# Kernel optimization log

Measured on AMD Instinct MI355X. Metric: run time of the kernel, lower is better.

Reference implementation:

```python
import jax, jax.numpy as jnp
import numpy as np


def _patches3x3(x):
    # x: [B,H,W,C] -> [B,H,W,9,C], SAME zero padding, patch index k = i*3+j
    B, H, W, C = x.shape
    p = jnp.pad(x, ((0, 0), (1, 1), (1, 1), (0, 0)))
    return jnp.stack([p[:, i:i + H, j:j + W, :] for i in range(3) for j in range(3)], axis=3)


def setup_inputs() -> dict:
    key = jax.random.key(0)
    k1, k2, k3 = jax.random.split(key, 3)
    B, H, W, CH, NC, DIM = 4, 80, 80, 256, 22, 256
    x = jax.random.normal(k1, (B, H, W, CH), dtype=jnp.float32)
    seg_mask = jax.random.uniform(k2, (B, H, W, NC), dtype=jnp.float32)
    # he_uniform over receptive field ch*3*3
    lim = np.sqrt(6.0 / (CH * 9)).astype(np.float32)
    conv_w = jax.random.uniform(k3, (CH, 3, 3, DIM), dtype=jnp.float32, minval=-lim, maxval=lim)
    return {"x": x, "seg_mask": seg_mask, "conv_w": conv_w}


def reference(x, seg_mask, conv_w):
    B, H, W, CH = x.shape
    NC = seg_mask.shape[-1]
    DIM = conv_w.shape[-1]
    # patches of segmentation map: [B,H,W,9,NC]
    s_patch = _patches3x3(seg_mask)
    m = seg_mask[:, :, :, None, :]                       # [B,H,W,1,NC]
    s_max = jnp.max(m, axis=-1, keepdims=True)           # [B,H,W,1,1]
    # keep patch values only for the argmax class at the center pixel
    sel = jnp.sum(jnp.where(m == s_max, s_patch, 0.0), axis=-1)  # [B,H,W,9]
    cnt = jnp.sum((sel != 0.0).astype(jnp.float32), axis=-1, keepdims=True)  # [B,H,W,1]
    norm = jnp.where(cnt > 0, 9.0 / jnp.maximum(cnt, 1.0), 0.0)  # divide_no_nan(9, cnt)
    # per-channel 3x3 patch extraction of features (== depthwise conv with eye(9))
    xp = _patches3x3(x)                                  # [B,H,W,9,CH]
    xp = xp * sel[..., None]                             # mask-gated patches
    w = conv_w.reshape(CH, 9, DIM)
    out = jnp.einsum('bhwkc,ckd->bhwd', xp, w) * norm    # [B,H,W,DIM]
    return out
```

## Files before the change

kernel.cpp:

```cpp
#include <hip/hip_runtime.h>
#include <hip/hip_bf16.h>
#include <cstdint>

#define B_ 4
#define H_ 80
#define W_ 80
#define CH_ 256
#define NC_ 22
#define DIM_ 256
#define NPIX (B_*H_*W_)

typedef unsigned short ushort;
typedef __attribute__((ext_vector_type(8))) short short8;
typedef __attribute__((ext_vector_type(4))) float floatx4;

static __device__ inline ushort f2bf(float v) {
    __hip_bfloat16 h = __float2bfloat16(v);
    ushort r;
    __builtin_memcpy(&r, &h, 2);
    return r;
}
static __device__ inline unsigned pk2(float a, float b) {
    return (unsigned)f2bf(a) | ((unsigned)f2bf(b) << 16);
}

__global__ __launch_bounds__(64) void sel_kernel(const float* __restrict__ seg,
                                                 float* __restrict__ ssel)
{
    int m = blockIdx.x * 64 + threadIdx.x;
    if (m >= NPIX) return;
    int w = m % W_;
    int h = (m / W_) % H_;
    int b = m / (W_ * H_);

    const float2* c2 = (const float2*)(seg + (size_t)m * NC_);
    float cv[NC_];
    #pragma unroll
    for (int c = 0; c < NC_ / 2; ++c) { float2 v = c2[c]; cv[2*c] = v.x; cv[2*c+1] = v.y; }
    float mx = -1e30f;
    #pragma unroll
    for (int c = 0; c < NC_; ++c) mx = fmaxf(mx, cv[c]);

    float sel[9];
    int cnt = 0;
    #pragma unroll
    for (int k = 0; k < 9; ++k) {
        int i = k / 3, j = k % 3;
        int hh = h + i - 1, ww = w + j - 1;
        float s = 0.f;
        if (hh >= 0 && hh < H_ && ww >= 0 && ww < W_) {
            const float2* n2 = (const float2*)(seg + ((size_t)((b * H_ + hh) * W_ + ww)) * NC_);
            #pragma unroll
            for (int c = 0; c < NC_ / 2; ++c) {
                float2 v = n2[c];
                s += (cv[2*c]   == mx) ? v.x : 0.f;
                s += (cv[2*c+1] == mx) ? v.y : 0.f;
            }
        }
        sel[k] = s;
        cnt += (s != 0.f) ? 1 : 0;
    }
    float norm = (cnt > 0) ? 9.f / (float)cnt : 0.f;
    #pragma unroll
    for (int k = 0; k < 9; ++k)
        ssel[k * NPIX + m] = sel[k] * norm;
}

__global__ __launch_bounds__(256) void cvt_w(const float* __restrict__ cw,
                                             ushort* __restrict__ wbT)
{
    __shared__ ushort ls[32][260];
    const int k  = blockIdx.x / 8;
    const int c0 = (blockIdx.x % 8) * 32;
    const int c   = threadIdx.x >> 3;
    const int seg = threadIdx.x & 7;

    const float* src = cw + ((size_t)(c0 + c) * 9 + k) * DIM_ + seg * 32;
    #pragma unroll
    for (int e = 0; e < 32; e += 4) {
        float4 v = *(const float4*)(src + e);
        unsigned* dst = (unsigned*)&ls[c][seg * 32 + e];
        dst[0] = pk2(v.x, v.y);
        dst[1] = pk2(v.z, v.w);
    }
    __syncthreads();

    const int d = threadIdx.x;
    ushort tmp[32];
    #pragma unroll
    for (int cc = 0; cc < 32; ++cc) tmp[cc] = ls[cc][d];
    uint4 o[4];
    __builtin_memcpy(o, tmp, 64);
    uint4* dst = (uint4*)(wbT + ((size_t)k * 256 + d) * 256 + c0);
    dst[0] = o[0]; dst[1] = o[1]; dst[2] = o[2]; dst[3] = o[3];
}

__global__ __launch_bounds__(256) void cvt_x(const float* __restrict__ x,
                                             ushort* __restrict__ xb)
{
    size_t idx = ((size_t)blockIdx.x * 256 + threadIdx.x) * 8;
    const float4* s = (const float4*)(x + idx);
    float4 a = s[0], b = s[1];
    uint4 o = make_uint4(pk2(a.x, a.y), pk2(a.z, a.w), pk2(b.x, b.y), pk2(b.z, b.w));
    *(uint4*)(xb + idx) = o;
}

template<bool XB16>
__global__ __launch_bounds__(256, 3) void conv2(const float* __restrict__ x,
                                                const ushort* __restrict__ xb,
                                                const float* __restrict__ ssel,
                                                const ushort* __restrict__ wbT,
                                                float* __restrict__ out)
{
    __shared__ ushort xsA[2][80 * 136];
    __shared__ float  sl[9][80];

    const int tid  = threadIdx.x;
    const int lane = tid & 63;
    const int wv   = tid >> 6;
    const int ln   = lane & 15;
    const int quad = lane >> 4;
    const int rt   = blockIdx.x;
    const int b    = rt / H_;
    const int h    = rt % H_;
    const int d0   = blockIdx.y * 128;

    int qm[5], qc[5];
    #pragma unroll
    for (int r = 0; r < 5; ++r) {
        int q = tid + 256 * r;
        qm[r] = q >> 4;
        qc[r] = q & 15;
    }

    for (int t = tid; t < 9 * 80; t += 256) {
        int k = t / 80, m = t - k * 80;
        sl[k][m] = ssel[k * NPIX + rt * W_ + m];
    }

    floatx4 O[5][2];
    #pragma unroll
    for (int i = 0; i < 5; ++i)
        #pragma unroll
        for (int jn = 0; jn < 2; ++jn)
            O[i][jn] = (floatx4){0.f, 0.f, 0.f, 0.f};

    uint4  sg[5];
    float4 fa[5], fb[5];
    bool   ok[5];

    auto stage_load = [&](int nit) {
        const int i   = nit / 6;
        const int rem = nit % 6;
        const int cc  = (rem / 3) * 128;
        const int jj  = rem % 3;
        const int rr  = h + i - 1;
        const bool rowok = (rr >= 0) && (rr < H_);
        const int rsafe = rowok ? rr : h;
        #pragma unroll
        for (int r = 0; r < 5; ++r) {
            const int col = qm[r] + jj - 1;
            const bool v = rowok && (col >= 0) && (col < W_);
            ok[r] = v;
            const size_t gp = ((size_t)(b * H_ + rsafe) * W_ + (v ? col : 0));
            if (XB16) {
                sg[r] = *(const uint4*)(xb + gp * CH_ + cc + qc[r] * 8);
            } else {
                const float* f = x + gp * CH_ + cc + qc[r] * 8;
                fa[r] = *(const float4*)f;
                fb[r] = *(const float4*)(f + 4);
            }
        }
    };
    auto stage_write = [&](int nit) {
        ushort* bp = xsA[nit & 1];
        #pragma unroll
        for (int r = 0; r < 5; ++r) {
            uint4 v;
            if (XB16) {
                v = ok[r] ? sg[r] : make_uint4(0u, 0u, 0u, 0u);
            } else {
                v = ok[r] ? make_uint4(pk2(fa[r].x, fa[r].y), pk2(fa[r].z, fa[r].w),
                                       pk2(fb[r].x, fb[r].y), pk2(fb[r].z, fb[r].w))
                          : make_uint4(0u, 0u, 0u, 0u);
            }
            *(uint4*)&bp[qm[r] * 136 + qc[r] * 8] = v;
        }
    };

    short8 Breg[8];
    auto loadB = [&](int nit) {
        const int i   = nit / 6;
        const int rem = nit % 6;
        const int cc  = (rem / 3) * 128;
        const int jj  = rem % 3;
        const int k   = 3 * i + jj;
        #pragma unroll
        for (int kk = 0; kk < 4; ++kk)
            #pragma unroll
            for (int jn = 0; jn < 2; ++jn)
                Breg[kk * 2 + jn] = *(const short8*)(wbT
                    + ((size_t)k * 256 + d0 + wv * 32 + jn * 16 + ln) * 256
                    + cc + kk * 32 + quad * 8);
    };

    stage_load(0);
    stage_write(0);
    loadB(0);
    __syncthreads();

    #pragma unroll 2
    for (int it = 0; it < 18; ++it) {
        const int i   = it / 6;
        const int rem = it % 6;
        const int jj  = rem % 3;
        const int k   = 3 * i + jj;
        const ushort* bp = xsA[it & 1];

        if (it < 17) stage_load(it + 1);

        floatx4 P[5][2];
        #pragma unroll
        for (int im = 0; im < 5; ++im)
            #pragma unroll
            for (int jn = 0; jn < 2; ++jn)
                P[im][jn] = (floatx4){0.f, 0.f, 0.f, 0.f};

        #pragma unroll
        for (int kk = 0; kk < 4; ++kk) {
            short8 a[5];
            #pragma unroll
            for (int im = 0; im < 5; ++im)
                a[im] = *(const short8*)&bp[(im * 16 + ln) * 136 + kk * 32 + quad * 8];
            #pragma unroll
            for (int im = 0; im < 5; ++im)
                #pragma unroll
                for (int jn = 0; jn < 2; ++jn)
                    P[im][jn] = __builtin_amdgcn_mfma_f32_16x16x32_bf16(
                        a[im], Breg[kk * 2 + jn], P[im][jn], 0, 0, 0);
        }

        if (it < 17) stage_write(it + 1);
        if (it < 17) loadB(it + 1);

        #pragma unroll
        for (int im = 0; im < 5; ++im) {
            const float4 sv = *(const float4*)&sl[k][im * 16 + quad * 4];
            #pragma unroll
            for (int jn = 0; jn < 2; ++jn) {
                O[im][jn][0] += sv.x * P[im][jn][0];
                O[im][jn][1] += sv.y * P[im][jn][1];
                O[im][jn][2] += sv.z * P[im][jn][2];
                O[im][jn][3] += sv.w * P[im][jn][3];
            }
        }
        __syncthreads();
    }

    #pragma unroll
    for (int im = 0; im < 5; ++im) {
        #pragma unroll
        for (int jn = 0; jn < 2; ++jn) {
            const int dd = d0 + wv * 32 + jn * 16 + ln;
            #pragma unroll
            for (int r = 0; r < 4; ++r) {
                const int m = im * 16 + quad * 4 + r;
                out[((size_t)(rt * W_ + m)) * DIM_ + dd] = O[im][jn][r];
            }
        }
    }
}

extern "C" void kernel_launch(void* const* d_in, const int* in_sizes, int n_in,
                              void* d_out, int out_size, void* d_ws, size_t ws_size,
                              hipStream_t stream)
{
    const float* x   = (const float*)d_in[0];
    const float* seg = (const float*)d_in[1];
    const float* cw  = (const float*)d_in[2];
    float* out = (float*)d_out;

    float*  ssel = (float*)d_ws;
    ushort* wbT  = (ushort*)((char*)d_ws + 921600);
    ushort* xb   = (ushort*)((char*)d_ws + 921600 + 1179648);
    const size_t need = 921600u + 1179648u + 13107200u;

    sel_kernel<<<dim3((NPIX + 63) / 64), dim3(64), 0, stream>>>(seg, ssel);
    cvt_w<<<dim3(72), dim3(256), 0, stream>>>(cw, wbT);

    if (ws_size >= need) {
        cvt_x<<<dim3(NPIX * CH_ / (256 * 8)), dim3(256), 0, stream>>>(x, xb);
        conv2<true><<<dim3(B_ * H_, 2), dim3(256), 0, stream>>>(x, xb, ssel, wbT, out);
    } else {
        conv2<false><<<dim3(B_ * H_, 2), dim3(256), 0, stream>>>(x, nullptr, ssel, wbT, out);
    }
}
```

Measured before the change: 158.2 us.

## Fuse prep kernels, compute selection in conv, stage rows once via global_load_lds

Merges weight and activation bf16 conversion into one prep launch and moves the segmentation selection computation into the conv kernel, which removes two launches and the ssel round trip. The conv kernel now stages each input row (84 columns with halo, zero-padding from a dedicated zero buffer) once per channel half using direct global-to-LDS loads with an XOR swizzle. The three horizontal taps reuse that tile by shifting rows, which cuts staging traffic threefold. In exchange, B fragments are loaded from global memory per tap without prefetch, the selection is recomputed twice (once per d-block), and the fallback path for small workspaces is gone.

Result: slower. 177.9 us (+12.5%).

```diff
diff --git a/kernel.cpp b/kernel.cpp
--- a/kernel.cpp
+++ b/kernel.cpp
@@ -24,62 +24,39 @@
     return (unsigned)f2bf(a) | ((unsigned)f2bf(b) << 16);
 }
 
-__global__ __launch_bounds__(64) void sel_kernel(const float* __restrict__ seg,
-                                                 float* __restrict__ ssel)
-{
-    int m = blockIdx.x * 64 + threadIdx.x;
-    if (m >= NPIX) return;
-    int w = m % W_;
-    int h = (m / W_) % H_;
-    int b = m / (W_ * H_);
-
-    const float2* c2 = (const float2*)(seg + (size_t)m * NC_);
-    float cv[NC_];
-    #pragma unroll
-    for (int c = 0; c < NC_ / 2; ++c) { float2 v = c2[c]; cv[2*c] = v.x; cv[2*c+1] = v.y; }
-    float mx = -1e30f;
-    #pragma unroll
-    for (int c = 0; c < NC_; ++c) mx = fmaxf(mx, cv[c]);
-
-    float sel[9];
-    int cnt = 0;
-    #pragma unroll
-    for (int k = 0; k < 9; ++k) {
-        int i = k / 3, j = k % 3;
-        int hh = h + i - 1, ww = w + j - 1;
-        float s = 0.f;
-        if (hh >= 0 && hh < H_ && ww >= 0 && ww < W_) {
-            const float2* n2 = (const float2*)(seg + ((size_t)((b * H_ + hh) * W_ + ww)) * NC_);
-            #pragma unroll
-            for (int c = 0; c < NC_ / 2; ++c) {
-                float2 v = n2[c];
-                s += (cv[2*c]   == mx) ? v.x : 0.f;
-                s += (cv[2*c+1] == mx) ? v.y : 0.f;
-            }
-        }
-        sel[k] = s;
-        cnt += (s != 0.f) ? 1 : 0;
-    }
-    float norm = (cnt > 0) ? 9.f / (float)cnt : 0.f;
-    #pragma unroll
-    for (int k = 0; k < 9; ++k)
-        ssel[k * NPIX + m] = sel[k] * norm;
-}
-
-__global__ __launch_bounds__(256) void cvt_w(const float* __restrict__ cw,
-                                             ushort* __restrict__ wbT)
+static __device__ inline void gll16(const ushort* g, ushort* l) {
+    __builtin_amdgcn_global_load_lds(
+        (const __attribute__((address_space(1))) unsigned int*)g,
+        (__attribute__((address_space(3))) unsigned int*)l, 16, 0, 0);
+}
+
+__global__ __launch_bounds__(256) void prep(const float* __restrict__ cw,
+                                            const float* __restrict__ x,
+                                            ushort* __restrict__ wbT,
+                                            ushort* __restrict__ xb)
 {
     __shared__ ushort ls[32][260];
+    if (blockIdx.x >= 72) {
+        const int bid = blockIdx.x - 72;
+        const size_t idx = ((size_t)bid * 256 + threadIdx.x) * 8;
+        const float4* s = (const float4*)(x + idx);
+        float4 a = s[0], b = s[1];
+        *(uint4*)(xb + idx) = make_uint4(pk2(a.x, a.y), pk2(a.z, a.w),
+                                         pk2(b.x, b.y), pk2(b.z, b.w));
+        if (bid == 0 && threadIdx.x < 64)
+            *(uint4*)(xb + (size_t)NPIX * CH_ + threadIdx.x * 8) = make_uint4(0, 0, 0, 0);
+        return;
+    }
     const int k  = blockIdx.x / 8;
     const int c0 = (blockIdx.x % 8) * 32;
     const int c   = threadIdx.x >> 3;
-    const int seg = threadIdx.x & 7;
-
-    const float* src = cw + ((size_t)(c0 + c) * 9 + k) * DIM_ + seg * 32;
+    const int sg  = threadIdx.x & 7;
+
+    const float* src = cw + ((size_t)(c0 + c) * 9 + k) * DIM_ + sg * 32;
     #pragma unroll
     for (int e = 0; e < 32; e += 4) {
         float4 v = *(const float4*)(src + e);
-        unsigned* dst = (unsigned*)&ls[c][seg * 32 + e];
+        unsigned* dst = (unsigned*)&ls[c][sg * 32 + e];
         dst[0] = pk2(v.x, v.y);
         dst[1] = pk2(v.z, v.w);
     }
@@ -95,24 +72,12 @@
     dst[0] = o[0]; dst[1] = o[1]; dst[2] = o[2]; dst[3] = o[3];
 }
 
-__global__ __launch_bounds__(256) void cvt_x(const float* __restrict__ x,
-                                             ushort* __restrict__ xb)
-{
-    size_t idx = ((size_t)blockIdx.x * 256 + threadIdx.x) * 8;
-    const float4* s = (const float4*)(x + idx);
-    float4 a = s[0], b = s[1];
-    uint4 o = make_uint4(pk2(a.x, a.y), pk2(a.z, a.w), pk2(b.x, b.y), pk2(b.z, b.w));
-    *(uint4*)(xb + idx) = o;
-}
-
-template<bool XB16>
-__global__ __launch_bounds__(256, 3) void conv2(const float* __restrict__ x,
-                                                const ushort* __restrict__ xb,
-                                                const float* __restrict__ ssel,
+__global__ __launch_bounds__(256, 3) void conv3(const ushort* __restrict__ xb,
+                                                const float* __restrict__ seg,
                                                 const ushort* __restrict__ wbT,
                                                 float* __restrict__ out)
 {
-    __shared__ ushort xsA[2][80 * 136];
+    __shared__ ushort xs[2][84 * 128];
     __shared__ float  sl[9][80];
 
     const int tid  = threadIdx.x;
@@ -120,138 +85,129 @@
     const int wv   = tid >> 6;
     const int ln   = lane & 15;
     const int quad = lane >> 4;
-    const int rt   = blockIdx.x;
+    const int d0   = blockIdx.x * 128;
+    const int rt   = blockIdx.y;
     const int b    = rt / H_;
     const int h    = rt % H_;
-    const int d0   = blockIdx.y * 128;
-
-    int qm[5], qc[5];
-    #pragma unroll
-    for (int r = 0; r < 5; ++r) {
-        int q = tid + 256 * r;
-        qm[r] = q >> 4;
-        qc[r] = q & 15;
-    }
-
-    for (int t = tid; t < 9 * 80; t += 256) {
-        int k = t / 80, m = t - k * 80;
-        sl[k][m] = ssel[k * NPIX + rt * W_ + m];
+    const ushort* zpad = xb + (size_t)NPIX * CH_;
+
+    const int rho0 = lane >> 4;
+    const int cp   = lane & 15;
+    auto stage = [&](int p, int buf) {
+        const int i  = p >> 1;
+        const int cc = (p & 1) * 128;
+        const int r  = h + i - 1;
+        const bool rowok = (r >= 0) && (r < H_);
+        for (int g = wv; g < 21; g += 4) {
+            const int rho = g * 4 + rho0;
+            const int scn = (cp & 8) | ((cp ^ rho) & 7);
+            const int col = rho - 1;
+            const bool v = rowok && (col >= 0) && (col < W_);
+            const ushort* src = v ? (xb + (((size_t)(b * H_ + r)) * W_ + col) * CH_
+                                        + cc + scn * 8)
+                                  : zpad;
+            gll16(src, &xs[buf][g * 512]);
+        }
+    };
+
+    stage(0, 0);
+
+    if (tid < W_) {
+        const int m = tid;
+        const float2* c2 = (const float2*)(seg + ((size_t)(b * H_ + h) * W_ + m) * NC_);
+        float cv[NC_];
+        #pragma unroll
+        for (int c = 0; c < NC_ / 2; ++c) { float2 v = c2[c]; cv[2*c] = v.x; cv[2*c+1] = v.y; }
+        float mx = -1e30f;
+        #pragma unroll
+        for (int c = 0; c < NC_; ++c) mx = fmaxf(mx, cv[c]);
+        float sel[9];
+        int cnt = 0;
+        #pragma unroll
+        for (int k = 0; k < 9; ++k) {
+            int i = k / 3, j = k % 3;
+            int hh = h + i - 1, ww = m + j - 1;
+            float s = 0.f;
+            if (hh >= 0 && hh < H_ && ww >= 0 && ww < W_) {
+                const float2* n2 = (const float2*)(seg + ((size_t)(b * H_ + hh) * W_ + ww) * NC_);
+                #pragma unroll
+                for (int c = 0; c < NC_ / 2; ++c) {
+                    float2 v = n2[c];
+                    s += (cv[2*c]   == mx) ? v.x : 0.f;
+                    s += (cv[2*c+1] == mx) ? v.y : 0.f;
+                }
+            }
+            sel[k] = s;
+            cnt += (s != 0.f) ? 1 : 0;
+        }
+        float norm = (cnt > 0) ? 9.f / (float)cnt : 0.f;
+        #pragma unroll
+        for (int k = 0; k < 9; ++k) sl[k][m] = sel[k] * norm;
     }
 
     floatx4 O[5][2];
     #pragma unroll
-    for (int i = 0; i < 5; ++i)
+    for (int im = 0; im < 5; ++im)
         #pragma unroll
         for (int jn = 0; jn < 2; ++jn)
-            O[i][jn] = (floatx4){0.f, 0.f, 0.f, 0.f};
-
-    uint4  sg[5];
-    float4 fa[5], fb[5];
-    bool   ok[5];
-
-    auto stage_load = [&](int nit) {
-        const int i   = nit / 6;
-        const int rem = nit % 6;
-        const int cc  = (rem / 3) * 128;
-        const int jj  = rem % 3;
-        const int rr  = h + i - 1;
-        const bool rowok = (rr >= 0) && (rr < H_);
-        const int rsafe = rowok ? rr : h;
-        #pragma unroll
-        for (int r = 0; r < 5; ++r) {
-            const int col = qm[r] + jj - 1;
-            const bool v = rowok && (col >= 0) && (col < W_);
-            ok[r] = v;
-            const size_t gp = ((size_t)(b * H_ + rsafe) * W_ + (v ? col : 0));
-            if (XB16) {
-                sg[r] = *(const uint4*)(xb + gp * CH_ + cc + qc[r] * 8);
-            } else {
-                const float* f = x + gp * CH_ + cc + qc[r] * 8;
-                fa[r] = *(const float4*)f;
-                fb[r] = *(const float4*)(f + 4);
-            }
-        }
-    };
-    auto stage_write = [&](int nit) {
-        ushort* bp = xsA[nit & 1];
-        #pragma unroll
-        for (int r = 0; r < 5; ++r) {
-            uint4 v;
-            if (XB16) {
-                v = ok[r] ? sg[r] : make_uint4(0u, 0u, 0u, 0u);
-            } else {
-                v = ok[r] ? make_uint4(pk2(fa[r].x, fa[r].y), pk2(fa[r].z, fa[r].w),
-                                       pk2(fb[r].x, fb[r].y), pk2(fb[r].z, fb[r].w))
-                          : make_uint4(0u, 0u, 0u, 0u);
-            }
-            *(uint4*)&bp[qm[r] * 136 + qc[r] * 8] = v;
-        }
-    };
-
-    short8 Breg[8];
-    auto loadB = [&](int nit) {
-        const int i   = nit / 6;
-        const int rem = nit % 6;
-        const int cc  = (rem / 3) * 128;
-        const int jj  = rem % 3;
-        const int k   = 3 * i + jj;
-        #pragma unroll
-        for (int kk = 0; kk < 4; ++kk)
-            #pragma unroll
-            for (int jn = 0; jn < 2; ++jn)
-                Breg[kk * 2 + jn] = *(const short8*)(wbT
-                    + ((size_t)k * 256 + d0 + wv * 32 + jn * 16 + ln) * 256
-                    + cc + kk * 32 + quad * 8);
-    };
-
-    stage_load(0);
-    stage_write(0);
-    loadB(0);
+            O[im][jn] = (floatx4){0.f, 0.f, 0.f, 0.f};
+
     __syncthreads();
 
-    #pragma unroll 2
-    for (int it = 0; it < 18; ++it) {
-        const int i   = it / 6;
-        const int rem = it % 6;
-        const int jj  = rem % 3;
-        const int k   = 3 * i + jj;
-        const ushort* bp = xsA[it & 1];
-
-        if (it < 17) stage_load(it + 1);
-
-        floatx4 P[5][2];
-        #pragma unroll
-        for (int im = 0; im < 5; ++im)
-            #pragma unroll
-            for (int jn = 0; jn < 2; ++jn)
-                P[im][jn] = (floatx4){0.f, 0.f, 0.f, 0.f};
-
-        #pragma unroll
-        for (int kk = 0; kk < 4; ++kk) {
-            short8 a[5];
+    for (int p = 0; p < 6; ++p) {
+        const int buf = p & 1;
+        const int i   = p >> 1;
+        const int cc  = (p & 1) * 128;
+        if (p < 5) stage(p + 1, buf ^ 1);
+
+        #pragma unroll
+        for (int j = 0; j < 3; ++j) {
+            const int k = 3 * i + j;
+
+            short8 Breg[8];
+            #pragma unroll
+            for (int kk = 0; kk < 4; ++kk)
+                #pragma unroll
+                for (int jn = 0; jn < 2; ++jn)
+                    Breg[kk * 2 + jn] = *(const short8*)(wbT
+                        + ((size_t)k * 256 + d0 + wv * 32 + jn * 16 + ln) * 256
+                        + cc + kk * 32 + quad * 8);
+
+            floatx4 P[5][2];
             #pragma unroll
             for (int im = 0; im < 5; ++im)
-                a[im] = *(const short8*)&bp[(im * 16 + ln) * 136 + kk * 32 + quad * 8];
-            #pragma unroll
-            for (int im = 0; im < 5; ++im)
                 #pragma unroll
                 for (int jn = 0; jn < 2; ++jn)
-                    P[im][jn] = __builtin_amdgcn_mfma_f32_16x16x32_bf16(
-                        a[im], Breg[kk * 2 + jn], P[im][jn], 0, 0, 0);
-        }
-
-        if (it < 17) stage_write(it + 1);
-        if (it < 17) loadB(it + 1);
-
-        #pragma unroll
-        for (int im = 0; im < 5; ++im) {
-            const float4 sv = *(const float4*)&sl[k][im * 16 + quad * 4];
-            #pragma unroll
-            for (int jn = 0; jn < 2; ++jn) {
-                O[im][jn][0] += sv.x * P[im][jn][0];
-                O[im][jn][1] += sv.y * P[im][jn][1];
-                O[im][jn][2] += sv.z * P[im][jn][2];
-                O[im][jn][3] += sv.w * P[im][jn][3];
+                    P[im][jn] = (floatx4){0.f, 0.f, 0.f, 0.f};
+
+            #pragma unroll
+            for (int kk = 0; kk < 4; ++kk) {
+                short8 a[5];
+                #pragma unroll
+                for (int im = 0; im < 5; ++im) {
+                    const int rho = im * 16 + ln + j;
+                    const int Gc  = 4 * kk + quad;
+                    const int ch  = (Gc & 8) | ((Gc ^ rho) & 7);
+                    a[im] = *(const short8*)&xs[buf][rho * 128 + ch * 8];
+                }
+                #pragma unroll
+                for (int im = 0; im < 5; ++im)
+                    #pragma unroll
+                    for (int jn = 0; jn < 2; ++jn)
+                        P[im][jn] = __builtin_amdgcn_mfma_f32_16x16x32_bf16(
+                            a[im], Breg[kk * 2 + jn], P[im][jn], 0, 0, 0);
+            }
+
+            #pragma unroll
+            for (int im = 0; im < 5; ++im) {
+                const floatx4 sv = *(const floatx4*)&sl[k][im * 16 + quad * 4];
+                #pragma unroll
+                for (int jn = 0; jn < 2; ++jn) {
+                    O[im][jn][0] += sv[0] * P[im][jn][0];
+                    O[im][jn][1] += sv[1] * P[im][jn][1];
+                    O[im][jn][2] += sv[2] * P[im][jn][2];
+                    O[im][jn][3] += sv[3] * P[im][jn][3];
+                }
             }
         }
         __syncthreads();
@@ -280,18 +236,9 @@
     const float* cw  = (const float*)d_in[2];
     float* out = (float*)d_out;
 
-    float*  ssel = (float*)d_ws;
-    ushort* wbT  = (ushort*)((char*)d_ws + 921600);
-    ushort* xb   = (ushort*)((char*)d_ws + 921600 + 1179648);
-    const size_t need = 921600u + 1179648u + 13107200u;
-
-    sel_kernel<<<dim3((NPIX + 63) / 64), dim3(64), 0, stream>>>(seg, ssel);
-    cvt_w<<<dim3(72), dim3(256), 0, stream>>>(cw, wbT);
-
-    if (ws_size >= need) {
-        cvt_x<<<dim3(NPIX * CH_ / (256 * 8)), dim3(256), 0, stream>>>(x, xb);
-        conv2<true><<<dim3(B_ * H_, 2), dim3(256), 0, stream>>>(x, xb, ssel, wbT, out);
-    } else {
-        conv2<false><<<dim3(B_ * H_, 2), dim3(256), 0, stream>>>(x, nullptr, ssel, wbT, out);
-    }
-}
+    ushort* wbT = (ushort*)d_ws;
+    ushort* xb  = (ushort*)((char*)d_ws + 1179648);
+
+    prep<<<dim3(72 + NPIX * CH_ / (256 * 8)), dim3(256), 0, stream>>>(cw, x, wbT, xb);
+    conv3<<<dim3(2, B_ * H_), dim3(256), 0, stream>>>(xb, seg, wbT, out);
+}
```

## Fuse selection, weight and input conversion, and conv into one persistent kernel

Applied to the files above, without the earlier changes.

Merges the selection-mask, weight-transpose, x-to-bf16 and MFMA conv kernels into a single 640-block launch. Blocks first do their share of the preprocessing, then meet at a software grid barrier built from per-block atomic flags in the workspace, and then run the conv tile. The aim is to remove three extra kernel launches and the gaps between them; the fp32-input fallback path is dropped. The barrier needs all blocks to be resident at once, and its flags are never reset, so later calls may pass the barrier without waiting. The design also assumes the workspace flags start in a usable state.

Result: slower. 245.1 us (+54.9%).

```diff
diff --git a/kernel.cpp b/kernel.cpp
--- a/kernel.cpp
+++ b/kernel.cpp
@@ -9,6 +9,7 @@
 #define NC_ 22
 #define DIM_ 256
 #define NPIX (B_*H_*W_)
+#define NBLK 640
 
 typedef unsigned short ushort;
 typedef __attribute__((ext_vector_type(8))) short short8;
@@ -24,130 +25,134 @@
     return (unsigned)f2bf(a) | ((unsigned)f2bf(b) << 16);
 }
 
-__global__ __launch_bounds__(64) void sel_kernel(const float* __restrict__ seg,
-                                                 float* __restrict__ ssel)
+__global__ __launch_bounds__(256, 3) void fused(const float* __restrict__ x,
+                                                const float* __restrict__ seg,
+                                                const float* __restrict__ cw,
+                                                float* __restrict__ out,
+                                                unsigned* __restrict__ sync,
+                                                float* __restrict__ ssel,
+                                                ushort* __restrict__ wbT,
+                                                ushort* __restrict__ xb)
 {
-    int m = blockIdx.x * 64 + threadIdx.x;
-    if (m >= NPIX) return;
-    int w = m % W_;
-    int h = (m / W_) % H_;
-    int b = m / (W_ * H_);
-
-    const float2* c2 = (const float2*)(seg + (size_t)m * NC_);
-    float cv[NC_];
-    #pragma unroll
-    for (int c = 0; c < NC_ / 2; ++c) { float2 v = c2[c]; cv[2*c] = v.x; cv[2*c+1] = v.y; }
-    float mx = -1e30f;
-    #pragma unroll
-    for (int c = 0; c < NC_; ++c) mx = fmaxf(mx, cv[c]);
-
-    float sel[9];
-    int cnt = 0;
-    #pragma unroll
-    for (int k = 0; k < 9; ++k) {
-        int i = k / 3, j = k % 3;
-        int hh = h + i - 1, ww = w + j - 1;
-        float s = 0.f;
-        if (hh >= 0 && hh < H_ && ww >= 0 && ww < W_) {
-            const float2* n2 = (const float2*)(seg + ((size_t)((b * H_ + hh) * W_ + ww)) * NC_);
-            #pragma unroll
-            for (int c = 0; c < NC_ / 2; ++c) {
-                float2 v = n2[c];
-                s += (cv[2*c]   == mx) ? v.x : 0.f;
-                s += (cv[2*c+1] == mx) ? v.y : 0.f;
+    __shared__ __align__(16) union {
+        ushort ls[32][260];
+        struct { ushort xsA[2][80 * 136]; float sl[9][80]; } c;
+    } U;
+
+    const int tid = threadIdx.x;
+    const int bid = blockIdx.x;
+
+    if (bid < 72) {
+        const int k  = bid / 8;
+        const int c0 = (bid % 8) * 32;
+        const int c  = tid >> 3;
+        const int sg = tid & 7;
+        const float* src = cw + ((size_t)(c0 + c) * 9 + k) * DIM_ + sg * 32;
+        #pragma unroll
+        for (int e = 0; e < 32; e += 4) {
+            float4 v = *(const float4*)(src + e);
+            unsigned* dst = (unsigned*)&U.ls[c][sg * 32 + e];
+            dst[0] = pk2(v.x, v.y);
+            dst[1] = pk2(v.z, v.w);
+        }
+        __syncthreads();
+        const int d = tid;
+        ushort tmp[32];
+        #pragma unroll
+        for (int cc2 = 0; cc2 < 32; ++cc2) tmp[cc2] = U.ls[cc2][d];
+        uint4 o[4];
+        __builtin_memcpy(o, tmp, 64);
+        uint4* dst = (uint4*)(wbT + ((size_t)k * 256 + d) * 256 + c0);
+        dst[0] = o[0]; dst[1] = o[1]; dst[2] = o[2]; dst[3] = o[3];
+    } else if (bid < 172) {
+        const int m = (bid - 72) * 256 + tid;
+        const int w = m % W_;
+        const int h = (m / W_) % H_;
+        const int b = m / (W_ * H_);
+        const float2* c2 = (const float2*)(seg + (size_t)m * NC_);
+        float cv[NC_];
+        #pragma unroll
+        for (int c = 0; c < NC_ / 2; ++c) { float2 v = c2[c]; cv[2*c] = v.x; cv[2*c+1] = v.y; }
+        float mx = -1e30f;
+        #pragma unroll
+        for (int c = 0; c < NC_; ++c) mx = fmaxf(mx, cv[c]);
+        float sel[9];
+        int cnt = 0;
+        #pragma unroll
+        for (int k = 0; k < 9; ++k) {
+            int i = k / 3, j = k % 3;
+            int hh = h + i - 1, ww = w + j - 1;
+            float s = 0.f;
+            if (hh >= 0 && hh < H_ && ww >= 0 && ww < W_) {
+                const float2* n2 = (const float2*)(seg + ((size_t)((b * H_ + hh) * W_ + ww)) * NC_);
+                #pragma unroll
+                for (int c = 0; c < NC_ / 2; ++c) {
+                    float2 v = n2[c];
+                    s += (cv[2*c]   == mx) ? v.x : 0.f;
+                    s += (cv[2*c+1] == mx) ? v.y : 0.f;
+                }
             }
-        }
-        sel[k] = s;
-        cnt += (s != 0.f) ? 1 : 0;
-    }
-    float norm = (cnt > 0) ? 9.f / (float)cnt : 0.f;
-    #pragma unroll
-    for (int k = 0; k < 9; ++k)
-        ssel[k * NPIX + m] = sel[k] * norm;
-}
-
-__global__ __launch_bounds__(256) void cvt_w(const float* __restrict__ cw,
-                                             ushort* __restrict__ wbT)
-{
-    __shared__ ushort ls[32][260];
-    const int k  = blockIdx.x / 8;
-    const int c0 = (blockIdx.x % 8) * 32;
-    const int c   = threadIdx.x >> 3;
-    const int seg = threadIdx.x & 7;
-
-    const float* src = cw + ((size_t)(c0 + c) * 9 + k) * DIM_ + seg * 32;
-    #pragma unroll
-    for (int e = 0; e < 32; e += 4) {
-        float4 v = *(const float4*)(src + e);
-        unsigned* dst = (unsigned*)&ls[c][seg * 32 + e];
-        dst[0] = pk2(v.x, v.y);
-        dst[1] = pk2(v.z, v.w);
-    }
+            sel[k] = s;
+            cnt += (s != 0.f) ? 1 : 0;
+        }
+        float norm = (cnt > 0) ? 9.f / (float)cnt : 0.f;
+        #pragma unroll
+        for (int k = 0; k < 9; ++k)
+            ssel[k * NPIX + m] = sel[k] * norm;
+    }
+    #pragma unroll
+    for (int u = 0; u < 5; ++u) {
+        const size_t idx = ((size_t)(bid + NBLK * u) * 256 + tid) * 8;
+        const float4* s = (const float4*)(x + idx);
+        float4 va = s[0], vb = s[1];
+        *(uint4*)(xb + idx) = make_uint4(pk2(va.x, va.y), pk2(va.z, va.w),
+                                         pk2(vb.x, vb.y), pk2(vb.z, vb.w));
+    }
+
     __syncthreads();
-
-    const int d = threadIdx.x;
-    ushort tmp[32];
-    #pragma unroll
-    for (int cc = 0; cc < 32; ++cc) tmp[cc] = ls[cc][d];
-    uint4 o[4];
-    __builtin_memcpy(o, tmp, 64);
-    uint4* dst = (uint4*)(wbT + ((size_t)k * 256 + d) * 256 + c0);
-    dst[0] = o[0]; dst[1] = o[1]; dst[2] = o[2]; dst[3] = o[3];
-}
-
-__global__ __launch_bounds__(256) void cvt_x(const float* __restrict__ x,
-                                             ushort* __restrict__ xb)
-{
-    size_t idx = ((size_t)blockIdx.x * 256 + threadIdx.x) * 8;
-    const float4* s = (const float4*)(x + idx);
-    float4 a = s[0], b = s[1];
-    uint4 o = make_uint4(pk2(a.x, a.y), pk2(a.z, a.w), pk2(b.x, b.y), pk2(b.z, b.w));
-    *(uint4*)(xb + idx) = o;
-}
-
-template<bool XB16>
-__global__ __launch_bounds__(256, 3) void conv2(const float* __restrict__ x,
-                                                const ushort* __restrict__ xb,
-                                                const float* __restrict__ ssel,
-                                                const ushort* __restrict__ wbT,
-                                                float* __restrict__ out)
-{
-    __shared__ ushort xsA[2][80 * 136];
-    __shared__ float  sl[9][80];
-
-    const int tid  = threadIdx.x;
+    if (tid == 0) { __threadfence(); atomicExch(&sync[1 + bid], 1u); }
+    if (bid == 0) {
+        for (int t = tid; t < NBLK; t += 256)
+            while (atomicAdd(&sync[1 + t], 0u) != 1u) __builtin_amdgcn_s_sleep(8);
+        __syncthreads();
+        if (tid == 0) { __threadfence(); atomicExch(&sync[0], 2u); }
+    }
+    if (tid == 0)
+        while (atomicAdd(&sync[0], 0u) != 2u) __builtin_amdgcn_s_sleep(8);
+    __threadfence();
+    __syncthreads();
+
     const int lane = tid & 63;
     const int wv   = tid >> 6;
     const int ln   = lane & 15;
     const int quad = lane >> 4;
-    const int rt   = blockIdx.x;
+    const int rt   = bid % 320;
+    const int d0   = (bid / 320) * 128;
     const int b    = rt / H_;
     const int h    = rt % H_;
-    const int d0   = blockIdx.y * 128;
 
     int qm[5], qc[5];
     #pragma unroll
     for (int r = 0; r < 5; ++r) {
-        int q = tid + 256 * r;
+        const int q = tid + 256 * r;
         qm[r] = q >> 4;
         qc[r] = q & 15;
     }
 
     for (int t = tid; t < 9 * 80; t += 256) {
         int k = t / 80, m = t - k * 80;
-        sl[k][m] = ssel[k * NPIX + rt * W_ + m];
+        U.c.sl[k][m] = ssel[k * NPIX + rt * W_ + m];
     }
 
     floatx4 O[5][2];
     #pragma unroll
-    for (int i = 0; i < 5; ++i)
+    for (int im = 0; im < 5; ++im)
         #pragma unroll
         for (int jn = 0; jn < 2; ++jn)
-            O[i][jn] = (floatx4){0.f, 0.f, 0.f, 0.f};
-
-    uint4  sg[5];
-    float4 fa[5], fb[5];
-    bool   ok[5];
+            O[im][jn] = (floatx4){0.f, 0.f, 0.f, 0.f};
+
+    uint4 sgv[5];
+    bool  ok[5];
 
     auto stage_load = [&](int nit) {
         const int i   = nit / 6;
@@ -156,34 +161,21 @@
         const int jj  = rem % 3;
         const int rr  = h + i - 1;
         const bool rowok = (rr >= 0) && (rr < H_);
-        const int rsafe = rowok ? rr : h;
         #pragma unroll
         for (int r = 0; r < 5; ++r) {
             const int col = qm[r] + jj - 1;
             const bool v = rowok && (col >= 0) && (col < W_);
             ok[r] = v;
-            const size_t gp = ((size_t)(b * H_ + rsafe) * W_ + (v ? col : 0));
-            if (XB16) {
-                sg[r] = *(const uint4*)(xb + gp * CH_ + cc + qc[r] * 8);
-            } else {
-                const float* f = x + gp * CH_ + cc + qc[r] * 8;
-                fa[r] = *(const float4*)f;
-                fb[r] = *(const float4*)(f + 4);
-            }
+            if (v)
+                sgv[r] = *(const uint4*)(xb + (((size_t)(b * H_ + rr)) * W_ + col) * CH_
+                                            + cc + qc[r] * 8);
         }
     };
     auto stage_write = [&](int nit) {
-        ushort* bp = xsA[nit & 1];
+        ushort* bp = U.c.xsA[nit & 1];
         #pragma unroll
         for (int r = 0; r < 5; ++r) {
-            uint4 v;
-            if (XB16) {
-                v = ok[r] ? sg[r] : make_uint4(0u, 0u, 0u, 0u);
-            } else {
-                v = ok[r] ? make_uint4(pk2(fa[r].x, fa[r].y), pk2(fa[r].z, fa[r].w),
-                                       pk2(fb[r].x, fb[r].y), pk2(fb[r].z, fb[r].w))
-                          : make_uint4(0u, 0u, 0u, 0u);
-            }
+            uint4 v = ok[r] ? sgv[r] : make_uint4(0u, 0u, 0u, 0u);
             *(uint4*)&bp[qm[r] * 136 + qc[r] * 8] = v;
         }
     };
@@ -215,7 +207,7 @@
         const int rem = it % 6;
         const int jj  = rem % 3;
         const int k   = 3 * i + jj;
-        const ushort* bp = xsA[it & 1];
+        const ushort* bp = U.c.xsA[it & 1];
 
         if (it < 17) stage_load(it + 1);
 
@@ -245,13 +237,13 @@
 
         #pragma unroll
         for (int im = 0; im < 5; ++im) {
-            const float4 sv = *(const float4*)&sl[k][im * 16 + quad * 4];
+            const floatx4 sv = *(const floatx4*)&U.c.sl[k][im * 16 + quad * 4];
             #pragma unroll
             for (int jn = 0; jn < 2; ++jn) {
-                O[im][jn][0] += sv.x * P[im][jn][0];
-                O[im][jn][1] += sv.y * P[im][jn][1];
-                O[im][jn][2] += sv.z * P[im][jn][2];
-                O[im][jn][3] += sv.w * P[im][jn][3];
+                O[im][jn][0] += sv[0] * P[im][jn][0];
+                O[im][jn][1] += sv[1] * P[im][jn][1];
+                O[im][jn][2] += sv[2] * P[im][jn][2];
+                O[im][jn][3] += sv[3] * P[im][jn][3];
             }
         }
         __syncthreads();
@@ -280,18 +272,10 @@
     const float* cw  = (const float*)d_in[2];
     float* out = (float*)d_out;
 
-    float*  ssel = (float*)d_ws;
-    ushort* wbT  = (ushort*)((char*)d_ws + 921600);
-    ushort* xb   = (ushort*)((char*)d_ws + 921600 + 1179648);
-    const size_t need = 921600u + 1179648u + 13107200u;
-
-    sel_kernel<<<dim3((NPIX + 63) / 64), dim3(64), 0, stream>>>(seg, ssel);
-    cvt_w<<<dim3(72), dim3(256), 0, stream>>>(cw, wbT);
-
-    if (ws_size >= need) {
-        cvt_x<<<dim3(NPIX * CH_ / (256 * 8)), dim3(256), 0, stream>>>(x, xb);
-        conv2<true><<<dim3(B_ * H_, 2), dim3(256), 0, stream>>>(x, xb, ssel, wbT, out);
-    } else {
-        conv2<false><<<dim3(B_ * H_, 2), dim3(256), 0, stream>>>(x, nullptr, ssel, wbT, out);
-    }
-}
+    unsigned* sync = (unsigned*)d_ws;
+    float*    ssel = (float*)((char*)d_ws + 4096);
+    ushort*   wbT  = (ushort*)((char*)d_ws + 4096 + 921600);
+    ushort*   xb   = (ushort*)((char*)d_ws + 4096 + 921600 + 1179648);
+
+    fused<<<dim3(NBLK), dim3(256), 0, stream>>>(x, seg, cw, out, sync, ssel, wbT, xb);
+}
```
